# Kernel optimization log

Measured on AMD Instinct MI355X. Metric: run time of the kernel, lower is better.

Reference implementation:

```python
import jax, jax.numpy as jnp
import numpy as np

HEADS = 16
DIM_HEAD = 64
SCALE = DIM_HEAD ** -0.5
LN_EPS = 1e-5


def setup_inputs() -> dict:
    key = jax.random.key(0)
    ks = jax.random.split(key, 4)
    B, N, D = 2, 2048, 1024
    inner = HEADS * DIM_HEAD  # 1024
    x = jax.random.normal(ks[0], (B, N, D), dtype=jnp.float32)
    m = jax.random.normal(ks[1], (B, N, N), dtype=jnp.float32)
    gamma = jnp.ones((D,), dtype=jnp.float32)
    beta = jnp.zeros((D,), dtype=jnp.float32)
    W_qkv = jax.random.normal(ks[2], (D, 3 * inner), dtype=jnp.float32) * (D ** -0.5)
    W_out = jax.random.normal(ks[3], (inner, D), dtype=jnp.float32) * (inner ** -0.5)
    return {"x": x, "m": m, "gamma": gamma, "beta": beta, "W_qkv": W_qkv, "W_out": W_out}


def reference(x, m, gamma, beta, W_qkv, W_out):
    B, N, D = x.shape
    # LayerNorm
    mu = jnp.mean(x, axis=-1, keepdims=True)
    var = jnp.var(x, axis=-1, keepdims=True)
    xn = (x - mu) * jax.lax.rsqrt(var + LN_EPS) * gamma + beta
    # QKV projection (no bias)
    qkv = xn @ W_qkv  # [B, N, 3*inner]
    q, k, v = jnp.split(qkv, 3, axis=-1)
    split_heads = lambda t: t.reshape(B, N, HEADS, DIM_HEAD).transpose(0, 2, 1, 3)  # b h n d
    q, k, v = split_heads(q), split_heads(k), split_heads(v)
    # Non-standard order: mask added BEFORE scaling
    qk = jnp.einsum('bhid,bhjd->bhij', q, k)
    dots = (qk + m[:, None, :, :]) * SCALE
    attn = jax.nn.softmax(dots, axis=-1)
    out = jnp.einsum('bhij,bhjd->bhid', attn, v)
    out = out.transpose(0, 2, 1, 3).reshape(B, N, HEADS * DIM_HEAD)
    return out @ W_out  # dropout is identity at inference
```

## Files before the change

### kernel.cpp

```cpp
#include <hip/hip_runtime.h>
#include <hip/hip_bf16.h>
#include <math.h>

typedef _Float16 f16;
typedef _Float16 f16x8 __attribute__((ext_vector_type(8)));
typedef float f32x4 __attribute__((ext_vector_type(4)));

#define HD 64
#define NH 16
#define BATCH 2
#define SEQ 2048
#define DMODEL 1024
#define NQKV 3072
#define ROWS 4096
#define NEG_BIG (-1.0e30f)

__device__ __forceinline__ f32x4 mfma16h(f16x8 a, f16x8 b, f32x4 c){
  return __builtin_amdgcn_mfma_f32_16x16x32_f16(a, b, c, 0, 0, 0);
}

__device__ __forceinline__ void gload16(const f16* g, f16* l){
  __builtin_amdgcn_global_load_lds(
      (const __attribute__((address_space(1))) unsigned int*)(g),
      (__attribute__((address_space(3))) unsigned int*)(l), 16, 0, 0);
}

__global__ __launch_bounds__(256) void ln_kernel(const float* __restrict__ x,
    const float* __restrict__ gamma, const float* __restrict__ beta,
    f16* __restrict__ xn)
{
  int row = blockIdx.x;
  int tid = threadIdx.x;
  const float* xr = x + (size_t)row * DMODEL;
  float v[4]; float s = 0.f, s2 = 0.f;
  #pragma unroll
  for (int i = 0; i < 4; i++){ float f = xr[tid + i*256]; v[i] = f; s += f; s2 += f*f; }
  #pragma unroll
  for (int off = 32; off; off >>= 1){ s += __shfl_xor(s, off); s2 += __shfl_xor(s2, off); }
  __shared__ float red[8];
  int wave = tid >> 6, lane = tid & 63;
  if (lane == 0){ red[wave] = s; red[4 + wave] = s2; }
  __syncthreads();
  s  = red[0] + red[1] + red[2] + red[3];
  s2 = red[4] + red[5] + red[6] + red[7];
  float mu  = s * (1.f / DMODEL);
  float var = s2 * (1.f / DMODEL) - mu * mu;
  float rs  = rsqrtf(var + 1e-5f);
  f16* xo = xn + (size_t)row * DMODEL;
  #pragma unroll
  for (int i = 0; i < 4; i++){
    int c = tid + i*256;
    xo[c] = (f16)((v[i] - mu) * rs * gamma[c] + beta[c]);
  }
}

__global__ __launch_bounds__(256) void transpose_f2h_kernel(const float* __restrict__ in,
    f16* __restrict__ out, int R, int C)
{
  __shared__ float t[32][33];
  int c0 = blockIdx.x * 32, r0 = blockIdx.y * 32;
  int lx = threadIdx.x & 31, ly = threadIdx.x >> 5;
  #pragma unroll
  for (int i = 0; i < 32; i += 8) t[ly + i][lx] = in[(size_t)(r0 + ly + i) * C + c0 + lx];
  __syncthreads();
  #pragma unroll
  for (int i = 0; i < 32; i += 8) out[(size_t)(c0 + ly + i) * R + r0 + lx] = (f16)t[lx][ly + i];
}

__global__ __launch_bounds__(256) void gemm_qkv(const f16* __restrict__ A,
    const float* __restrict__ W, f16* __restrict__ Qo, f16* __restrict__ Ko,
    f16* __restrict__ Vo)
{
  __shared__ __align__(16) f16 As[128][40];
  __shared__ __align__(16) f16 Bs[128][40];
  const int K = DMODEL, N = NQKV;
  int bm = blockIdx.y * 128, bn = blockIdx.x * 128;
  int tid = threadIdx.x;
  int wave = tid >> 6, lane = tid & 63, quad = lane >> 4, l15 = lane & 15;
  int mw = (wave >> 1) * 64, nw = (wave & 1) * 64;
  int srow = tid >> 2, schunk = tid & 3;
  int kr = tid >> 3;
  int g  = tid & 7;

  f32x4 zero = {0.f, 0.f, 0.f, 0.f};
  f32x4 acc[4][4];
  #pragma unroll
  for (int i = 0; i < 4; i++)
    #pragma unroll
    for (int j = 0; j < 4; j++) acc[i][j] = zero;

  for (int k0 = 0; k0 < K; k0 += 32){
    __syncthreads();
    uint4 a0 = *(const uint4*)(A + (size_t)(bm + srow     ) * K + k0 + schunk*8);
    uint4 a1 = *(const uint4*)(A + (size_t)(bm + srow + 64) * K + k0 + schunk*8);
    float4 w[4];
    #pragma unroll
    for (int o = 0; o < 4; o++)
      w[o] = *(const float4*)(W + (size_t)(k0 + kr) * N + bn + o*32 + g*4);
    *(uint4*)&As[srow     ][schunk*8] = a0;
    *(uint4*)&As[srow + 64][schunk*8] = a1;
    #pragma unroll
    for (int o = 0; o < 4; o++){
      Bs[o*32 + g*4 + 0][kr] = (f16)w[o].x;
      Bs[o*32 + g*4 + 1][kr] = (f16)w[o].y;
      Bs[o*32 + g*4 + 2][kr] = (f16)w[o].z;
      Bs[o*32 + g*4 + 3][kr] = (f16)w[o].w;
    }
    __syncthreads();

    f16x8 af[4], bfr[4];
    #pragma unroll
    for (int i = 0; i < 4; i++) af[i]  = *(const f16x8*)&As[mw + i*16 + l15][quad*8];
    #pragma unroll
    for (int i = 0; i < 4; i++) bfr[i] = *(const f16x8*)&Bs[nw + i*16 + l15][quad*8];
    #pragma unroll
    for (int mi = 0; mi < 4; mi++)
      #pragma unroll
      for (int ni = 0; ni < 4; ni++)
        acc[mi][ni] = mfma16h(af[mi], bfr[ni], acc[mi][ni]);
  }

  #pragma unroll
  for (int mi = 0; mi < 4; mi++){
    #pragma unroll
    for (int ni = 0; ni < 4; ni++){
      #pragma unroll
      for (int reg = 0; reg < 4; reg++){
        int r = bm + mw + mi*16 + quad*4 + reg;
        int c = bn + nw + ni*16 + l15;
        float v = acc[mi][ni][reg];
        int which = c >> 10;
        int hc = c & 1023;
        int h = hc >> 6, d = hc & 63;
        int b = r >> 11, nseq = r & 2047;
        size_t bh = (size_t)(b * NH + h);
        if (which == 0)      Qo[(bh * SEQ + nseq) * HD + d] = (f16)v;
        else if (which == 1) Ko[(bh * SEQ + nseq) * HD + d] = (f16)v;
        else                 Vo[(bh * HD + d) * SEQ + nseq] = (f16)v;
      }
    }
  }
}

__global__ __launch_bounds__(256) void gemm_out(const f16* __restrict__ A,
    const f16* __restrict__ Bt, float* __restrict__ C, int M, int N, int K)
{
  __shared__ __align__(16) f16 As[128][40];
  __shared__ __align__(16) f16 Bs[128][40];
  int bm = blockIdx.y * 128, bn = blockIdx.x * 128;
  int tid = threadIdx.x;
  int wave = tid >> 6, lane = tid & 63, quad = lane >> 4, l15 = lane & 15;
  int mw = (wave >> 1) * 64, nw = (wave & 1) * 64;
  int srow = tid >> 2, schunk = tid & 3;

  f32x4 zero = {0.f, 0.f, 0.f, 0.f};
  f32x4 acc[4][4];
  #pragma unroll
  for (int i = 0; i < 4; i++)
    #pragma unroll
    for (int j = 0; j < 4; j++) acc[i][j] = zero;

  for (int k0 = 0; k0 < K; k0 += 32){
    __syncthreads();
    uint4 a0 = *(const uint4*)(A  + (size_t)(bm + srow     ) * K + k0 + schunk*8);
    uint4 a1 = *(const uint4*)(A  + (size_t)(bm + srow + 64) * K + k0 + schunk*8);
    uint4 b0 = *(const uint4*)(Bt + (size_t)(bn + srow     ) * K + k0 + schunk*8);
    uint4 b1 = *(const uint4*)(Bt + (size_t)(bn + srow + 64) * K + k0 + schunk*8);
    *(uint4*)&As[srow     ][schunk*8] = a0;
    *(uint4*)&As[srow + 64][schunk*8] = a1;
    *(uint4*)&Bs[srow     ][schunk*8] = b0;
    *(uint4*)&Bs[srow + 64][schunk*8] = b1;
    __syncthreads();

    f16x8 af[4], bfr[4];
    #pragma unroll
    for (int i = 0; i < 4; i++) af[i]  = *(const f16x8*)&As[mw + i*16 + l15][quad*8];
    #pragma unroll
    for (int i = 0; i < 4; i++) bfr[i] = *(const f16x8*)&Bs[nw + i*16 + l15][quad*8];
    #pragma unroll
    for (int mi = 0; mi < 4; mi++)
      #pragma unroll
      for (int ni = 0; ni < 4; ni++)
        acc[mi][ni] = mfma16h(af[mi], bfr[ni], acc[mi][ni]);
  }

  #pragma unroll
  for (int mi = 0; mi < 4; mi++)
    #pragma unroll
    for (int ni = 0; ni < 4; ni++)
      #pragma unroll
      for (int reg = 0; reg < 4; reg++){
        int r = bm + mw + mi*16 + quad*4 + reg;
        int c = bn + nw + ni*16 + l15;
        C[(size_t)r * N + c] = acc[mi][ni][reg];
      }
}

__global__ __launch_bounds__(256, 4) void attn_kernel(const f16* __restrict__ Q,
    const f16* __restrict__ Kb, const f16* __restrict__ Vt,
    const float* __restrict__ mask, f16* __restrict__ Ao)
{
  __shared__ __align__(16) f16 KsB[2][64*64];
  __shared__ __align__(16) f16 VsB[2][64*64];
  __shared__ __align__(16) f16 Ps[4*16*64];

  int bh = blockIdx.y; int b = bh >> 4; int h = bh & 15;
  int q0 = blockIdx.x * 64;
  int tid = threadIdx.x;
  int wave = tid >> 6, lane = tid & 63, quad = lane >> 4, l15 = lane & 15;

  int rA = (wave*2 + 0)*8 + (lane >> 3);
  int rB = (wave*2 + 1)*8 + (lane >> 3);
  int cp = lane & 7;
  int ccA = cp ^ (rA & 7);
  int ccB = cp ^ (rB & 7);
  const f16* Kg = Kb + (size_t)bh * SEQ * HD;
  const f16* Vg = Vt + (size_t)bh * HD * SEQ;
  f16* ldsKA = &KsB[0][0] + (wave*2 + 0)*8*64;
  f16* ldsKB = &KsB[0][0] + (wave*2 + 1)*8*64;
  f16* ldsVA = &VsB[0][0] + (wave*2 + 0)*8*64;
  f16* ldsVB = &VsB[0][0] + (wave*2 + 1)*8*64;

  f16x8 qf[2];
  {
    const f16* qrow = Q + ((size_t)bh * SEQ + q0 + wave*16 + l15) * HD + quad*8;
    qf[0] = *(const f16x8*)(qrow);
    qf[1] = *(const f16x8*)(qrow + 32);
  }

  const float* mbase = mask + ((size_t)b * SEQ + q0 + wave*16) * SEQ;

  gload16(Kg + (size_t)(0 + rA)*HD + ccA*8, ldsKA);
  gload16(Kg + (size_t)(0 + rB)*HD + ccB*8, ldsKB);
  gload16(Vg + (size_t)rA*SEQ + 0 + ccA*8, ldsVA);
  gload16(Vg + (size_t)rB*SEQ + 0 + ccB*8, ldsVB);

  f32x4 zero = {0.f, 0.f, 0.f, 0.f};
  f32x4 O[4];
  #pragma unroll
  for (int nt = 0; nt < 4; nt++) O[nt] = zero;
  float mrun[4], lrun[4];
  #pragma unroll
  for (int r = 0; r < 4; r++){ mrun[r] = NEG_BIG; lrun[r] = 0.f; }

  const int NT = SEQ / 64;
  for (int it = 0; it < NT; ++it){
    int cur = it & 1;
    int j0 = it * 64;
    asm volatile("s_waitcnt vmcnt(0)" ::: "memory");
    __syncthreads();
    if (it + 1 < NT){
      int nb = cur ^ 1;
      int j0n = j0 + 64;
      gload16(Kg + (size_t)(j0n + rA)*HD + ccA*8, ldsKA + nb*4096);
      gload16(Kg + (size_t)(j0n + rB)*HD + ccB*8, ldsKB + nb*4096);
      gload16(Vg + (size_t)rA*SEQ + j0n + ccA*8, ldsVA + nb*4096);
      gload16(Vg + (size_t)rB*SEQ + j0n + ccB*8, ldsVB + nb*4096);
    }
    const f16* Ksc = &KsB[cur][0];
    const f16* Vsc = &VsB[cur][0];

    float sv[4][4];
    __builtin_amdgcn_s_setprio(1);
    #pragma unroll
    for (int jt = 0; jt < 4; jt++){
      f32x4 a = zero;
      int r = jt*16 + l15;
      #pragma unroll
      for (int kk = 0; kk < 2; kk++){
        int c = kk*4 + quad;
        f16x8 kf = *(const f16x8*)&Ksc[r*64 + ((c ^ (r & 7))*8)];
        a = mfma16h(qf[kk], kf, a);
      }
      #pragma unroll
      for (int reg = 0; reg < 4; reg++){
        float mv = mbase[(size_t)(quad*4 + reg)*SEQ + j0 + jt*16 + l15];
        sv[jt][reg] = (a[reg] + mv) * 0.125f;
      }
    }
    __builtin_amdgcn_s_setprio(0);

    #pragma unroll
    for (int reg = 0; reg < 4; reg++){
      float t = fmaxf(fmaxf(sv[0][reg], sv[1][reg]), fmaxf(sv[2][reg], sv[3][reg]));
      #pragma unroll
      for (int off = 1; off <= 8; off <<= 1) t = fmaxf(t, __shfl_xor(t, off));
      float nm = fmaxf(mrun[reg], t);
      float alpha = __expf(mrun[reg] - nm);
      mrun[reg] = nm;
      float ps = 0.f;
      #pragma unroll
      for (int jt = 0; jt < 4; jt++){
        float p = __expf(sv[jt][reg] - nm);
        sv[jt][reg] = p; ps += p;
      }
      #pragma unroll
      for (int off = 1; off <= 8; off <<= 1) ps += __shfl_xor(ps, off);
      lrun[reg] = lrun[reg] * alpha + ps;
      #pragma unroll
      for (int nt = 0; nt < 4; nt++) O[nt][reg] *= alpha;
    }

    #pragma unroll
    for (int jt = 0; jt < 4; jt++)
      #pragma unroll
      for (int reg = 0; reg < 4; reg++){
        int q = quad*4 + reg;
        Ps[wave*1024 + q*64 + (((jt*2 + (l15 >> 3)) ^ (q & 7))*8) + (l15 & 7)]
            = (f16)sv[jt][reg];
      }

    __builtin_amdgcn_s_setprio(1);
    #pragma unroll
    for (int nt = 0; nt < 4; nt++){
      #pragma unroll
      for (int kk = 0; kk < 2; kk++){
        int c = kk*4 + quad;
        int rv = nt*16 + l15;
        f16x8 pf = *(const f16x8*)&Ps[wave*1024 + l15*64 + ((c ^ (l15 & 7))*8)];
        f16x8 vf = *(const f16x8*)&Vsc[rv*64 + ((c ^ (rv & 7))*8)];
        O[nt] = mfma16h(pf, vf, O[nt]);
      }
    }
    __builtin_amdgcn_s_setprio(0);
  }

  #pragma unroll
  for (int nt = 0; nt < 4; nt++){
    #pragma unroll
    for (int reg = 0; reg < 4; reg++){
      float o = O[nt][reg] / lrun[reg];
      int r = q0 + wave*16 + quad*4 + reg;
      Ao[((size_t)(b * SEQ + r)) * DMODEL + h * HD + nt*16 + l15] = (f16)o;
    }
  }
}

extern "C" void kernel_launch(void* const* d_in, const int* in_sizes, int n_in,
                              void* d_out, int out_size, void* d_ws, size_t ws_size,
                              hipStream_t stream)
{
  (void)in_sizes; (void)n_in; (void)out_size; (void)ws_size;
  const float* x     = (const float*)d_in[0];
  const float* m     = (const float*)d_in[1];
  const float* gamma = (const float*)d_in[2];
  const float* beta  = (const float*)d_in[3];
  const float* Wqkv  = (const float*)d_in[4];
  const float* Wout  = (const float*)d_in[5];
  float* out = (float*)d_out;

  char* ws = (char*)d_ws;
  f16* xn    = (f16*)(ws + 0);
  f16* Ao    = (f16*)(ws + 0);
  f16* Qb    = (f16*)(ws + 8388608);
  f16* WoutT = (f16*)(ws + 8388608);
  f16* Kbuf  = (f16*)(ws + 16777216);
  f16* Vtb   = (f16*)(ws + 25165824);

  ln_kernel<<<ROWS, 256, 0, stream>>>(x, gamma, beta, xn);
  gemm_qkv<<<dim3(NQKV/128, ROWS/128), 256, 0, stream>>>(xn, Wqkv, Qb, Kbuf, Vtb);
  attn_kernel<<<dim3(SEQ/64, BATCH*NH), 256, 0, stream>>>(Qb, Kbuf, Vtb, m, Ao);
  transpose_f2h_kernel<<<dim3(DMODEL/32, DMODEL/32), 256, 0, stream>>>(Wout, WoutT, DMODEL, DMODEL);
  gemm_out<<<dim3(DMODEL/128, ROWS/128), 256, 0, stream>>>(Ao, WoutT, out, ROWS, DMODEL, DMODEL);
}
```

Baseline: 298.1 us.

## Double-buffer GEMMs with async LDS loads, transposed operands, and lazy softmax rescale

Both GEMMs now stage A and B tiles into double-buffered, XOR-swizzled LDS through global_load_lds, so the next K-slice loads while the current one is computed. The QKV weight is first transposed and converted to fp16 by a separate kernel so that gemm_qkv reads contiguous fp16 rows. The attention kernel swaps the MFMA operands so that each lane owns one query row and can read the mask as a contiguous float4. It also switches softmax to exp2 with a folded scale and skips the running-max rescale unless the max grows by more than 8. LayerNorm is vectorized with float4 loads and f16x4 stores. This adds an extra transpose launch and more workspace, and the lazy rescale lets unnormalized probabilities grow up to 2^8, which could affect fp16 precision.

After: 270.2 us. -9.3%, faster.

```diff
diff --git a/kernel.cpp b/kernel.cpp
--- a/kernel.cpp
+++ b/kernel.cpp
@@ -3,6 +3,7 @@
 #include <math.h>
 
 typedef _Float16 f16;
+typedef _Float16 f16x4 __attribute__((ext_vector_type(4)));
 typedef _Float16 f16x8 __attribute__((ext_vector_type(8)));
 typedef float f32x4 __attribute__((ext_vector_type(4)));
 
@@ -14,6 +15,7 @@
 #define NQKV 3072
 #define ROWS 4096
 #define NEG_BIG (-1.0e30f)
+#define SCALE_LOG2E 0.18033688011112042f
 
 __device__ __forceinline__ f32x4 mfma16h(f16x8 a, f16x8 b, f32x4 c){
   return __builtin_amdgcn_mfma_f32_16x16x32_f16(a, b, c, 0, 0, 0);
@@ -31,10 +33,9 @@
 {
   int row = blockIdx.x;
   int tid = threadIdx.x;
-  const float* xr = x + (size_t)row * DMODEL;
-  float v[4]; float s = 0.f, s2 = 0.f;
-  #pragma unroll
-  for (int i = 0; i < 4; i++){ float f = xr[tid + i*256]; v[i] = f; s += f; s2 += f*f; }
+  float4 v = ((const float4*)(x + (size_t)row * DMODEL))[tid];
+  float s  = v.x + v.y + v.z + v.w;
+  float s2 = v.x*v.x + v.y*v.y + v.z*v.z + v.w*v.w;
   #pragma unroll
   for (int off = 32; off; off >>= 1){ s += __shfl_xor(s, off); s2 += __shfl_xor(s2, off); }
   __shared__ float red[8];
@@ -46,12 +47,14 @@
   float mu  = s * (1.f / DMODEL);
   float var = s2 * (1.f / DMODEL) - mu * mu;
   float rs  = rsqrtf(var + 1e-5f);
-  f16* xo = xn + (size_t)row * DMODEL;
-  #pragma unroll
-  for (int i = 0; i < 4; i++){
-    int c = tid + i*256;
-    xo[c] = (f16)((v[i] - mu) * rs * gamma[c] + beta[c]);
-  }
+  float4 g  = ((const float4*)gamma)[tid];
+  float4 be = ((const float4*)beta)[tid];
+  f16x4 o;
+  o[0] = (f16)((v.x - mu) * rs * g.x + be.x);
+  o[1] = (f16)((v.y - mu) * rs * g.y + be.y);
+  o[2] = (f16)((v.z - mu) * rs * g.z + be.z);
+  o[3] = (f16)((v.w - mu) * rs * g.w + be.w);
+  *(f16x4*)(xn + (size_t)row * DMODEL + tid*4) = o;
 }
 
 __global__ __launch_bounds__(256) void transpose_f2h_kernel(const float* __restrict__ in,
@@ -67,20 +70,34 @@
   for (int i = 0; i < 32; i += 8) out[(size_t)(c0 + ly + i) * R + r0 + lx] = (f16)t[lx][ly + i];
 }
 
-__global__ __launch_bounds__(256) void gemm_qkv(const f16* __restrict__ A,
-    const float* __restrict__ W, f16* __restrict__ Qo, f16* __restrict__ Ko,
+
+__global__ __launch_bounds__(256, 3) void gemm_qkv(const f16* __restrict__ A,
+    const f16* __restrict__ Bt, f16* __restrict__ Qo, f16* __restrict__ Ko,
     f16* __restrict__ Vo)
 {
-  __shared__ __align__(16) f16 As[128][40];
-  __shared__ __align__(16) f16 Bs[128][40];
-  const int K = DMODEL, N = NQKV;
+  __shared__ __align__(16) f16 As[2][128][32];
+  __shared__ __align__(16) f16 Bs[2][128][32];
+  const int K = DMODEL;
   int bm = blockIdx.y * 128, bn = blockIdx.x * 128;
   int tid = threadIdx.x;
   int wave = tid >> 6, lane = tid & 63, quad = lane >> 4, l15 = lane & 15;
   int mw = (wave >> 1) * 64, nw = (wave & 1) * 64;
-  int srow = tid >> 2, schunk = tid & 3;
-  int kr = tid >> 3;
-  int g  = tid & 7;
+
+  int sr0 = wave*16 + (lane >> 2);
+  int sr1 = sr0 + 64;
+  int sc  = (lane & 3) ^ (sr0 & 3);
+  const f16* Ag = A  + (size_t)bm * K;
+  const f16* Bg = Bt + (size_t)bn * K;
+  f16* ldsA0 = &As[0][wave*16     ][0];
+  f16* ldsA1 = &As[0][wave*16 + 64][0];
+  f16* ldsB0 = &Bs[0][wave*16     ][0];
+  f16* ldsB1 = &Bs[0][wave*16 + 64][0];
+
+#define QSTAGE(buf, k0) do{ \
+    gload16(Ag + (size_t)sr0 * K + (k0) + sc*8, ldsA0 + (buf)*4096); \
+    gload16(Ag + (size_t)sr1 * K + (k0) + sc*8, ldsA1 + (buf)*4096); \
+    gload16(Bg + (size_t)sr0 * K + (k0) + sc*8, ldsB0 + (buf)*4096); \
+    gload16(Bg + (size_t)sr1 * K + (k0) + sc*8, ldsB1 + (buf)*4096); }while(0)
 
   f32x4 zero = {0.f, 0.f, 0.f, 0.f};
   f32x4 acc[4][4];
@@ -89,36 +106,28 @@
     #pragma unroll
     for (int j = 0; j < 4; j++) acc[i][j] = zero;
 
-  for (int k0 = 0; k0 < K; k0 += 32){
+  QSTAGE(0, 0);
+  const int NS = K / 32;
+  for (int it = 0; it < NS; ++it){
+    int cur = it & 1;
+    asm volatile("s_waitcnt vmcnt(0)" ::: "memory");
     __syncthreads();
-    uint4 a0 = *(const uint4*)(A + (size_t)(bm + srow     ) * K + k0 + schunk*8);
-    uint4 a1 = *(const uint4*)(A + (size_t)(bm + srow + 64) * K + k0 + schunk*8);
-    float4 w[4];
-    #pragma unroll
-    for (int o = 0; o < 4; o++)
-      w[o] = *(const float4*)(W + (size_t)(k0 + kr) * N + bn + o*32 + g*4);
-    *(uint4*)&As[srow     ][schunk*8] = a0;
-    *(uint4*)&As[srow + 64][schunk*8] = a1;
-    #pragma unroll
-    for (int o = 0; o < 4; o++){
-      Bs[o*32 + g*4 + 0][kr] = (f16)w[o].x;
-      Bs[o*32 + g*4 + 1][kr] = (f16)w[o].y;
-      Bs[o*32 + g*4 + 2][kr] = (f16)w[o].z;
-      Bs[o*32 + g*4 + 3][kr] = (f16)w[o].w;
-    }
-    __syncthreads();
-
+    if (it + 1 < NS) QSTAGE(cur ^ 1, (it + 1) * 32);
+    int ca = (quad ^ (l15 & 3)) * 8;
     f16x8 af[4], bfr[4];
     #pragma unroll
-    for (int i = 0; i < 4; i++) af[i]  = *(const f16x8*)&As[mw + i*16 + l15][quad*8];
-    #pragma unroll
-    for (int i = 0; i < 4; i++) bfr[i] = *(const f16x8*)&Bs[nw + i*16 + l15][quad*8];
+    for (int i = 0; i < 4; i++) af[i]  = *(const f16x8*)&As[cur][mw + i*16 + l15][ca];
+    #pragma unroll
+    for (int i = 0; i < 4; i++) bfr[i] = *(const f16x8*)&Bs[cur][nw + i*16 + l15][ca];
+    __builtin_amdgcn_s_setprio(1);
     #pragma unroll
     for (int mi = 0; mi < 4; mi++)
       #pragma unroll
       for (int ni = 0; ni < 4; ni++)
         acc[mi][ni] = mfma16h(af[mi], bfr[ni], acc[mi][ni]);
-  }
+    __builtin_amdgcn_s_setprio(0);
+  }
+#undef QSTAGE
 
   #pragma unroll
   for (int mi = 0; mi < 4; mi++){
@@ -142,16 +151,31 @@
   }
 }
 
-__global__ __launch_bounds__(256) void gemm_out(const f16* __restrict__ A,
+__global__ __launch_bounds__(256, 3) void gemm_out(const f16* __restrict__ A,
     const f16* __restrict__ Bt, float* __restrict__ C, int M, int N, int K)
 {
-  __shared__ __align__(16) f16 As[128][40];
-  __shared__ __align__(16) f16 Bs[128][40];
+  __shared__ __align__(16) f16 As[2][128][32];
+  __shared__ __align__(16) f16 Bs[2][128][32];
   int bm = blockIdx.y * 128, bn = blockIdx.x * 128;
   int tid = threadIdx.x;
   int wave = tid >> 6, lane = tid & 63, quad = lane >> 4, l15 = lane & 15;
   int mw = (wave >> 1) * 64, nw = (wave & 1) * 64;
-  int srow = tid >> 2, schunk = tid & 3;
+
+  int sr0 = wave*16 + (lane >> 2);
+  int sr1 = sr0 + 64;
+  int sc  = (lane & 3) ^ (sr0 & 3);
+  const f16* Ag = A  + (size_t)bm * K;
+  const f16* Bg = Bt + (size_t)bn * K;
+  f16* ldsA0 = &As[0][wave*16     ][0];
+  f16* ldsA1 = &As[0][wave*16 + 64][0];
+  f16* ldsB0 = &Bs[0][wave*16     ][0];
+  f16* ldsB1 = &Bs[0][wave*16 + 64][0];
+
+#define OSTAGE(buf, k0) do{ \
+    gload16(Ag + (size_t)sr0 * K + (k0) + sc*8, ldsA0 + (buf)*4096); \
+    gload16(Ag + (size_t)sr1 * K + (k0) + sc*8, ldsA1 + (buf)*4096); \
+    gload16(Bg + (size_t)sr0 * K + (k0) + sc*8, ldsB0 + (buf)*4096); \
+    gload16(Bg + (size_t)sr1 * K + (k0) + sc*8, ldsB1 + (buf)*4096); }while(0)
 
   f32x4 zero = {0.f, 0.f, 0.f, 0.f};
   f32x4 acc[4][4];
@@ -160,29 +184,28 @@
     #pragma unroll
     for (int j = 0; j < 4; j++) acc[i][j] = zero;
 
-  for (int k0 = 0; k0 < K; k0 += 32){
+  OSTAGE(0, 0);
+  const int NS = 1024 / 32;
+  for (int it = 0; it < NS; ++it){
+    int cur = it & 1;
+    asm volatile("s_waitcnt vmcnt(0)" ::: "memory");
     __syncthreads();
-    uint4 a0 = *(const uint4*)(A  + (size_t)(bm + srow     ) * K + k0 + schunk*8);
-    uint4 a1 = *(const uint4*)(A  + (size_t)(bm + srow + 64) * K + k0 + schunk*8);
-    uint4 b0 = *(const uint4*)(Bt + (size_t)(bn + srow     ) * K + k0 + schunk*8);
-    uint4 b1 = *(const uint4*)(Bt + (size_t)(bn + srow + 64) * K + k0 + schunk*8);
-    *(uint4*)&As[srow     ][schunk*8] = a0;
-    *(uint4*)&As[srow + 64][schunk*8] = a1;
-    *(uint4*)&Bs[srow     ][schunk*8] = b0;
-    *(uint4*)&Bs[srow + 64][schunk*8] = b1;
-    __syncthreads();
-
+    if (it + 1 < NS) OSTAGE(cur ^ 1, (it + 1) * 32);
+    int ca = (quad ^ (l15 & 3)) * 8;
     f16x8 af[4], bfr[4];
     #pragma unroll
-    for (int i = 0; i < 4; i++) af[i]  = *(const f16x8*)&As[mw + i*16 + l15][quad*8];
-    #pragma unroll
-    for (int i = 0; i < 4; i++) bfr[i] = *(const f16x8*)&Bs[nw + i*16 + l15][quad*8];
+    for (int i = 0; i < 4; i++) af[i]  = *(const f16x8*)&As[cur][mw + i*16 + l15][ca];
+    #pragma unroll
+    for (int i = 0; i < 4; i++) bfr[i] = *(const f16x8*)&Bs[cur][nw + i*16 + l15][ca];
+    __builtin_amdgcn_s_setprio(1);
     #pragma unroll
     for (int mi = 0; mi < 4; mi++)
       #pragma unroll
       for (int ni = 0; ni < 4; ni++)
         acc[mi][ni] = mfma16h(af[mi], bfr[ni], acc[mi][ni]);
-  }
+    __builtin_amdgcn_s_setprio(0);
+  }
+#undef OSTAGE
 
   #pragma unroll
   for (int mi = 0; mi < 4; mi++)
@@ -228,7 +251,7 @@
     qf[1] = *(const f16x8*)(qrow + 32);
   }
 
-  const float* mbase = mask + ((size_t)b * SEQ + q0 + wave*16) * SEQ;
+  const float* mrow = mask + ((size_t)b * SEQ + q0 + wave*16 + l15) * SEQ + quad*4;
 
   gload16(Kg + (size_t)(0 + rA)*HD + ccA*8, ldsKA);
   gload16(Kg + (size_t)(0 + rB)*HD + ccB*8, ldsKB);
@@ -239,9 +262,7 @@
   f32x4 O[4];
   #pragma unroll
   for (int nt = 0; nt < 4; nt++) O[nt] = zero;
-  float mrun[4], lrun[4];
-  #pragma unroll
-  for (int r = 0; r < 4; r++){ mrun[r] = NEG_BIG; lrun[r] = 0.f; }
+  float mrun = NEG_BIG, lrun = 0.f;
 
   const int NT = SEQ / 64;
   for (int it = 0; it < NT; ++it){
@@ -268,68 +289,83 @@
       int r = jt*16 + l15;
       #pragma unroll
       for (int kk = 0; kk < 2; kk++){
-        int c = kk*4 + quad;
-        f16x8 kf = *(const f16x8*)&Ksc[r*64 + ((c ^ (r & 7))*8)];
-        a = mfma16h(qf[kk], kf, a);
+        f16x8 kf = *(const f16x8*)&Ksc[r*64 + (((kk*4 + quad) ^ (r & 7))*8)];
+        a = mfma16h(kf, qf[kk], a);
       }
+      float4 mv = *(const float4*)(mrow + j0 + jt*16);
+      sv[jt][0] = (a[0] + mv.x) * SCALE_LOG2E;
+      sv[jt][1] = (a[1] + mv.y) * SCALE_LOG2E;
+      sv[jt][2] = (a[2] + mv.z) * SCALE_LOG2E;
+      sv[jt][3] = (a[3] + mv.w) * SCALE_LOG2E;
+    }
+    __builtin_amdgcn_s_setprio(0);
+
+    float m0 = fmaxf(fmaxf(sv[0][0], sv[0][1]), fmaxf(sv[0][2], sv[0][3]));
+    float m1 = fmaxf(fmaxf(sv[1][0], sv[1][1]), fmaxf(sv[1][2], sv[1][3]));
+    float m2 = fmaxf(fmaxf(sv[2][0], sv[2][1]), fmaxf(sv[2][2], sv[2][3]));
+    float m3 = fmaxf(fmaxf(sv[3][0], sv[3][1]), fmaxf(sv[3][2], sv[3][3]));
+    float tmax = fmaxf(fmaxf(m0, m1), fmaxf(m2, m3));
+    tmax = fmaxf(tmax, __shfl_xor(tmax, 16));
+    tmax = fmaxf(tmax, __shfl_xor(tmax, 32));
+
+    if (__any(tmax > mrun + 8.f)){
+      float nm = fmaxf(mrun, tmax);
+      float alpha = exp2f(mrun - nm);
+      mrun = nm;
+      lrun *= alpha;
+      float aR[4];
+      #pragma unroll
+      for (int reg = 0; reg < 4; reg++)
+        aR[reg] = __shfl(alpha, (lane & 48) | (quad*4 + reg));
+      #pragma unroll
+      for (int nt = 0; nt < 4; nt++)
+        #pragma unroll
+        for (int reg = 0; reg < 4; reg++) O[nt][reg] *= aR[reg];
+    }
+
+    float ps = 0.f;
+    #pragma unroll
+    for (int jt = 0; jt < 4; jt++)
       #pragma unroll
       for (int reg = 0; reg < 4; reg++){
-        float mv = mbase[(size_t)(quad*4 + reg)*SEQ + j0 + jt*16 + l15];
-        sv[jt][reg] = (a[reg] + mv) * 0.125f;
-      }
-    }
-    __builtin_amdgcn_s_setprio(0);
-
-    #pragma unroll
-    for (int reg = 0; reg < 4; reg++){
-      float t = fmaxf(fmaxf(sv[0][reg], sv[1][reg]), fmaxf(sv[2][reg], sv[3][reg]));
-      #pragma unroll
-      for (int off = 1; off <= 8; off <<= 1) t = fmaxf(t, __shfl_xor(t, off));
-      float nm = fmaxf(mrun[reg], t);
-      float alpha = __expf(mrun[reg] - nm);
-      mrun[reg] = nm;
-      float ps = 0.f;
-      #pragma unroll
-      for (int jt = 0; jt < 4; jt++){
-        float p = __expf(sv[jt][reg] - nm);
+        float p = exp2f(sv[jt][reg] - mrun);
         sv[jt][reg] = p; ps += p;
       }
-      #pragma unroll
-      for (int off = 1; off <= 8; off <<= 1) ps += __shfl_xor(ps, off);
-      lrun[reg] = lrun[reg] * alpha + ps;
-      #pragma unroll
-      for (int nt = 0; nt < 4; nt++) O[nt][reg] *= alpha;
-    }
-
-    #pragma unroll
-    for (int jt = 0; jt < 4; jt++)
-      #pragma unroll
-      for (int reg = 0; reg < 4; reg++){
-        int q = quad*4 + reg;
-        Ps[wave*1024 + q*64 + (((jt*2 + (l15 >> 3)) ^ (q & 7))*8) + (l15 & 7)]
-            = (f16)sv[jt][reg];
-      }
+    ps += __shfl_xor(ps, 16);
+    ps += __shfl_xor(ps, 32);
+    lrun += ps;
+
+    #pragma unroll
+    for (int jt = 0; jt < 4; jt++){
+      f16x4 ph;
+      ph[0] = (f16)sv[jt][0]; ph[1] = (f16)sv[jt][1];
+      ph[2] = (f16)sv[jt][2]; ph[3] = (f16)sv[jt][3];
+      *(f16x4*)&Ps[wave*1024 + l15*64 + (((jt*2 + (quad>>1)) ^ (l15 & 7))*8) + (quad & 1)*4] = ph;
+    }
 
     __builtin_amdgcn_s_setprio(1);
     #pragma unroll
     for (int nt = 0; nt < 4; nt++){
       #pragma unroll
       for (int kk = 0; kk < 2; kk++){
-        int c = kk*4 + quad;
         int rv = nt*16 + l15;
-        f16x8 pf = *(const f16x8*)&Ps[wave*1024 + l15*64 + ((c ^ (l15 & 7))*8)];
-        f16x8 vf = *(const f16x8*)&Vsc[rv*64 + ((c ^ (rv & 7))*8)];
+        f16x8 pf = *(const f16x8*)&Ps[wave*1024 + l15*64 + (((kk*4 + quad) ^ (l15 & 7))*8)];
+        f16x8 vf = *(const f16x8*)&Vsc[rv*64 + (((kk*4 + quad) ^ (rv & 7))*8)];
         O[nt] = mfma16h(pf, vf, O[nt]);
       }
     }
     __builtin_amdgcn_s_setprio(0);
   }
 
+  float lR[4];
+  #pragma unroll
+  for (int reg = 0; reg < 4; reg++)
+    lR[reg] = __shfl(lrun, (lane & 48) | (quad*4 + reg));
   #pragma unroll
   for (int nt = 0; nt < 4; nt++){
     #pragma unroll
     for (int reg = 0; reg < 4; reg++){
-      float o = O[nt][reg] / lrun[reg];
+      float o = O[nt][reg] / lR[reg];
       int r = q0 + wave*16 + quad*4 + reg;
       Ao[((size_t)(b * SEQ + r)) * DMODEL + h * HD + nt*16 + l15] = (f16)o;
     }
@@ -356,9 +392,11 @@
   f16* WoutT = (f16*)(ws + 8388608);
   f16* Kbuf  = (f16*)(ws + 16777216);
   f16* Vtb   = (f16*)(ws + 25165824);
+  f16* WqkvT = (f16*)(ws + 33554432);
 
   ln_kernel<<<ROWS, 256, 0, stream>>>(x, gamma, beta, xn);
-  gemm_qkv<<<dim3(NQKV/128, ROWS/128), 256, 0, stream>>>(xn, Wqkv, Qb, Kbuf, Vtb);
+  transpose_f2h_kernel<<<dim3(NQKV/32, DMODEL/32), 256, 0, stream>>>(Wqkv, WqkvT, DMODEL, NQKV);
+  gemm_qkv<<<dim3(NQKV/128, ROWS/128), 256, 0, stream>>>(xn, WqkvT, Qb, Kbuf, Vtb);
   attn_kernel<<<dim3(SEQ/64, BATCH*NH), 256, 0, stream>>>(Qb, Kbuf, Vtb, m, Ao);
   transpose_f2h_kernel<<<dim3(DMODEL/32, DMODEL/32), 256, 0, stream>>>(Wout, WoutT, DMODEL, DMODEL);
   gemm_out<<<dim3(DMODEL/128, ROWS/128), 256, 0, stream>>>(Ao, WoutT, out, ROWS, DMODEL, DMODEL);
```
